# Kernel tuning notes

Hardware: AMD Instinct MI355X
Metric: run time of the kernel (lower is better)

Reference implementation:

```python
import jax, jax.numpy as jnp
import numpy as np

B, N, D = 2, 2048, 1024
H = 16
HD = D // H  # head_dim for kq and v

def setup_inputs() -> dict:
    key = jax.random.key(0)
    ks = jax.random.split(key, 5)
    scale = 1.0 / np.sqrt(D)
    return {
        "x": jax.random.normal(ks[0], (B, N, D), dtype=jnp.float32),
        "Wq": jax.random.normal(ks[1], (D, D), dtype=jnp.float32) * scale,
        "Wk": jax.random.normal(ks[2], (D, D), dtype=jnp.float32) * scale,
        "Wv": jax.random.normal(ks[3], (D, D), dtype=jnp.float32) * scale,
        "Wo": jax.random.normal(ks[4], (D, D), dtype=jnp.float32) * scale,
        "bo": jnp.zeros((D,), dtype=jnp.float32),
    }

def reference(x, Wq, Wk, Wv, Wo, bo):
    b, n, _ = x.shape
    # projections; torch Linear computes x @ W.T
    q = (x @ Wq.T).reshape(b, n, H, HD).transpose(0, 2, 1, 3)  # [B,H,N,HD]
    k = (x @ Wk.T).reshape(b, n, H, HD).transpose(0, 2, 1, 3)
    v = (x @ Wv.T).reshape(b, n, H, HD).transpose(0, 2, 1, 3)
    scores = jnp.einsum('bhqd,bhkd->bhqk', q, k) / jnp.sqrt(jnp.asarray(HD, x.dtype))
    causal = jnp.tril(jnp.ones((n, n), dtype=bool))
    scores = jnp.where(causal, scores, jnp.asarray(-jnp.inf, scores.dtype))
    probs = jax.nn.softmax(scores, axis=-1)  # dropout p=0.0 (eval)
    out = jnp.einsum('bhqk,bhkd->bhqd', probs, v)  # [B,H,N,HD]
    out = out.transpose(0, 2, 1, 3).reshape(b, n, D)
    return out @ Wo.T + bo
```

## Files before the change

kernel.cpp:

```cpp
#include <hip/hip_runtime.h>
#include <hip/hip_bf16.h>


typedef __bf16 bf16;
typedef __bf16 bf16x2 __attribute__((ext_vector_type(2)));
typedef __bf16 bf16x4 __attribute__((ext_vector_type(4)));
typedef __bf16 bf16x8 __attribute__((ext_vector_type(8)));
typedef float f32x4 __attribute__((ext_vector_type(4)));
typedef unsigned int u32x4 __attribute__((ext_vector_type(4)));

__device__ __forceinline__ f32x4 mfma16(bf16x8 a, bf16x8 b, f32x4 c) {
    return __builtin_amdgcn_mfma_f32_16x16x32_bf16(a, b, c, 0, 0, 0);
}

__device__ __forceinline__ void gload16(const bf16* g, bf16* l) {
    __builtin_amdgcn_global_load_lds(
        (const __attribute__((address_space(1))) unsigned int*)g,
        (__attribute__((address_space(3))) unsigned int*)l, 16, 0, 0);
}

__device__ __forceinline__ unsigned pk2(float a, float b) {
    bf16x2 v;
    v[0] = (bf16)a;
    v[1] = (bf16)b;
    return __builtin_bit_cast(unsigned, v);
}

__global__ __launch_bounds__(256) void f2b_kernel(const float* __restrict__ in,
                                                  bf16* __restrict__ out, int n) {
    int i = (blockIdx.x * 256 + threadIdx.x) * 4;
    if (i >= n) return;
    float4 v = *(const float4*)&in[i];
    bf16x4 o;
    o.x = (bf16)v.x; o.y = (bf16)v.y; o.z = (bf16)v.z; o.w = (bf16)v.w;
    *(bf16x4*)&out[i] = o;
}

__global__ __launch_bounds__(256) void w2b_kernel(
    const float* __restrict__ w0, const float* __restrict__ w1,
    const float* __restrict__ w2, const float* __restrict__ w3,
    bf16* __restrict__ o0, bf16* __restrict__ o1,
    bf16* __restrict__ o2, bf16* __restrict__ o3) {
    int sel = blockIdx.x >> 10;
    const float* in = sel == 0 ? w0 : sel == 1 ? w1 : sel == 2 ? w2 : w3;
    bf16* out = sel == 0 ? o0 : sel == 1 ? o1 : sel == 2 ? o2 : o3;
    int i = ((blockIdx.x & 1023) * 256 + threadIdx.x) * 4;
    float4 v = *(const float4*)&in[i];
    bf16x4 o;
    o.x = (bf16)v.x; o.y = (bf16)v.y; o.z = (bf16)v.z; o.w = (bf16)v.w;
    *(bf16x4*)&out[i] = o;
}

template <int MODE>
__device__ __forceinline__ void gemm_body(const bf16* __restrict__ A,
                                          const bf16* __restrict__ B,
                                          bf16* __restrict__ Cb,
                                          float* __restrict__ Cf,
                                          const float* __restrict__ bias,
                                          float scale, int N, int K, int row0, int col0) {
    __shared__ alignas(16) bf16 sA[128 * 32];
    __shared__ alignas(16) bf16 sB[128 * 32];
    const int tid  = threadIdx.x;
    const int lane = tid & 63;
    const int wave = tid >> 6;
    const int wrow = (wave >> 1) * 64;
    const int wcol = (wave & 1) * 64;
    const int la = lane & 15, lb = lane >> 4;

    const f32x4 fzero = {0.f, 0.f, 0.f, 0.f};
    f32x4 acc[4][4];
#pragma unroll
    for (int m = 0; m < 4; ++m)
#pragma unroll
        for (int n = 0; n < 4; ++n) acc[m][n] = fzero;

    for (int k0 = 0; k0 < K; k0 += 32) {
#pragma unroll
        for (int i = 0; i < 2; ++i) {
            int idx = i * 256 + tid;
            int r = idx >> 2, s = idx & 3;
            gload16(&A[(size_t)(row0 + r) * K + k0 + s * 8], &sA[idx * 8]);
            gload16(&B[(size_t)(col0 + r) * K + k0 + s * 8], &sB[idx * 8]);
        }
        __syncthreads();
        bf16x8 af[4], bfv[4];
#pragma unroll
        for (int m = 0; m < 4; ++m)
            af[m] = *(const bf16x8*)&sA[(wrow + m * 16 + la) * 32 + lb * 8];
#pragma unroll
        for (int n = 0; n < 4; ++n)
            bfv[n] = *(const bf16x8*)&sB[(wcol + n * 16 + la) * 32 + lb * 8];
#pragma unroll
        for (int m = 0; m < 4; ++m)
#pragma unroll
            for (int n = 0; n < 4; ++n)
                acc[m][n] = mfma16(af[m], bfv[n], acc[m][n]);
        __syncthreads();
    }
#pragma unroll
    for (int m = 0; m < 4; ++m)
#pragma unroll
        for (int n = 0; n < 4; ++n) {
            int col = col0 + wcol + n * 16 + la;
            if (MODE == 2) {
                int hh = col >> 6, hd = col & 63;
                int hc = hd >> 4, lav = hd & 15;
                int sp = row0 + wrow + m * 16 + lb * 4;
                int ktile = sp >> 6, k = sp & 63;
                int c = k >> 4, g = (k >> 2) & 3;
                size_t addr = (size_t)(ktile * 16 + hh) * 4096 +
                              (size_t)((hc * 2 + (c >> 1)) * 512 +
                                       (lav + g * 16) * 8 + (c & 1) * 4);
                bf16x4 o4;
#pragma unroll
                for (int r = 0; r < 4; ++r) o4[r] = (bf16)acc[m][n][r];
                *(bf16x4*)&Cb[addr] = o4;
            } else if (MODE == 3) {
                int hh = col >> 6, hd = col & 63;
#pragma unroll
                for (int r = 0; r < 4; ++r) {
                    int row = row0 + wrow + m * 16 + lb * 4 + r;
                    int ktile = row >> 6, key = row & 63;
                    size_t addr = (size_t)(ktile * 16 + hh) * 4096 +
                                  (size_t)(((key >> 4) * 2 + (hd >> 5)) * 512 +
                                           ((key & 15) + ((hd >> 3) & 3) * 16) * 8 +
                                           (hd & 7));
                    Cb[addr] = (bf16)acc[m][n][r];
                }
            } else {
#pragma unroll
                for (int r = 0; r < 4; ++r) {
                    int row = row0 + wrow + m * 16 + lb * 4 + r;
                    if (MODE == 1)
                        Cf[(size_t)row * N + col] = acc[m][n][r] + bias[col];
                    else
                        Cb[(size_t)row * N + col] = (bf16)(acc[m][n][r] * scale);
                }
            }
        }
}

__global__ __launch_bounds__(256) void gemm_qkv_kernel(
    const bf16* __restrict__ xb, const bf16* __restrict__ wq,
    const bf16* __restrict__ wk, const bf16* __restrict__ wv,
    bf16* __restrict__ Q, bf16* __restrict__ Kf, bf16* __restrict__ Vf) {
    int z = blockIdx.z;
    if (z == 2) {
        gemm_body<2>(xb, wv, Vf, nullptr, nullptr, 1.f, 1024, 1024,
                     blockIdx.x * 128, blockIdx.y * 128);
    } else if (z == 1) {
        gemm_body<3>(xb, wk, Kf, nullptr, nullptr, 1.f, 1024, 1024,
                     blockIdx.x * 128, blockIdx.y * 128);
    } else {
        gemm_body<0>(xb, wq, Q, nullptr, nullptr, 0.1803368801111204f, 1024, 1024,
                     blockIdx.x * 128, blockIdx.y * 128);
    }
}

__global__ __launch_bounds__(256) void gemm_out_kernel(
    const bf16* __restrict__ att, const bf16* __restrict__ wo,
    float* __restrict__ out, const float* __restrict__ bias) {
    gemm_body<1>(att, wo, nullptr, out, bias, 1.f, 1024, 1024,
                 blockIdx.x * 128, blockIdx.y * 128);
}

__global__ __launch_bounds__(256, 2) void attn_kernel(
    const bf16* __restrict__ Q, const bf16* __restrict__ Kf,
    const bf16* __restrict__ Vf, bf16* __restrict__ O) {
    __shared__ alignas(16) char smem[32768];
    const int lane = threadIdx.x & 63;
    const int wave = threadIdx.x >> 6;
    const int bid = blockIdx.x;
    const int bh = (bid & 7) * 4 + ((bid >> 3) & 3);
    const int slot = bid >> 5;
    const int qt = slot < 8 ? slot : 23 - slot;
    const int h = bh & 15;
    const int b = bh >> 4;
    const int q0w = qt * 128 + wave * 32;
    const int rowbase = b * 2048;
    const int la = lane & 15, lb = lane >> 4;
    const f32x4 fzero = {0.f, 0.f, 0.f, 0.f};
    const float C = 14.426950408889634f;
    const int colbase = h * 64;
    const size_t TSTRIDE = 16 * 4096;

    const bf16* kg = Kf + ((size_t)(b * 32) * 16 + h) * 4096 + lane * 8;
    const bf16* vg = Vf + ((size_t)(b * 32) * 16 + h) * 4096 + lane * 8;

    bf16x8 aq[2][2];
#pragma unroll
    for (int mf = 0; mf < 2; ++mf) {
        const bf16* qp = &Q[(size_t)(rowbase + q0w + mf * 16 + la) * 1024 + colbase];
#pragma unroll
        for (int kc = 0; kc < 2; ++kc) aq[mf][kc] = *(const bf16x8*)(qp + kc * 32 + lb * 8);
    }

    bf16x8 bones;
#pragma unroll
    for (int j = 0; j < 8; ++j) bones[j] = (bf16)1.0f;

    f32x4 o[2][4], lacc[2];
#pragma unroll
    for (int mf = 0; mf < 2; ++mf) {
        lacc[mf] = fzero;
#pragma unroll
        for (int hc = 0; hc < 4; ++hc) o[mf][hc] = fzero;
    }

    const int nt = (q0w + 95) >> 6;
    const int ntmax = 2 * qt + 2;

    auto STAGE = [&](int tile, int cur) {
        const bf16* ks = kg + (size_t)tile * TSTRIDE;
        const bf16* vs = vg + (size_t)tile * TSTRIDE;
        char* dst = smem + cur * 16384;
#pragma unroll
        for (int i = 0; i < 2; ++i) {
            int f = wave + i * 4;
            gload16(ks + f * 512, (bf16*)(dst + f * 1024));
            gload16(vs + f * 512, (bf16*)(dst + 8192 + f * 1024));
        }
    };

    STAGE(0, 0);
    __syncthreads();

    int cur = 0;
    for (int t = 0; t < ntmax; ++t) {
        if (t + 1 < ntmax) STAGE(t + 1, cur ^ 1);
        if (t < nt) {
            const char* kbuf = smem + cur * 16384;
            const char* vbuf = kbuf + 8192;
            f32x4 s[2][4];
#pragma unroll
            for (int mf = 0; mf < 2; ++mf)
#pragma unroll
                for (int ck = 0; ck < 4; ++ck) s[mf][ck] = fzero;
            __builtin_amdgcn_s_setprio(1);
#pragma unroll
            for (int ck = 0; ck < 4; ++ck) {
                bf16x8 k0 = *(const bf16x8*)(kbuf + (ck * 2 + 0) * 1024 + lane * 16);
                bf16x8 k1 = *(const bf16x8*)(kbuf + (ck * 2 + 1) * 1024 + lane * 16);
#pragma unroll
                for (int mf = 0; mf < 2; ++mf) {
                    s[mf][ck] = mfma16(k0, aq[mf][0], s[mf][ck]);
                    s[mf][ck] = mfma16(k1, aq[mf][1], s[mf][ck]);
                }
            }
            __builtin_amdgcn_s_setprio(0);
            if (t == nt - 1) {
                const int k0r = t * 64;
#pragma unroll
                for (int mf = 0; mf < 2; ++mf) {
                    int qrow = q0w + mf * 16 + la;
#pragma unroll
                    for (int ck = 0; ck < 4; ++ck)
#pragma unroll
                        for (int r = 0; r < 4; ++r) {
                            int key = k0r + ck * 16 + lb * 4 + r;
                            if (key > qrow) s[mf][ck][r] = -1e30f;
                        }
                }
            }
            bf16x8 pa[2][2];
#pragma unroll
            for (int mf = 0; mf < 2; ++mf) {
                unsigned pk[4][2];
#pragma unroll
                for (int ck = 0; ck < 4; ++ck) {
                    float p0 = __builtin_amdgcn_exp2f(s[mf][ck][0] - C);
                    float p1 = __builtin_amdgcn_exp2f(s[mf][ck][1] - C);
                    float p2 = __builtin_amdgcn_exp2f(s[mf][ck][2] - C);
                    float p3 = __builtin_amdgcn_exp2f(s[mf][ck][3] - C);
                    pk[ck][0] = pk2(p0, p1);
                    pk[ck][1] = pk2(p2, p3);
                }
#pragma unroll
                for (int kc2 = 0; kc2 < 2; ++kc2) {
                    u32x4 w;
                    w.x = pk[kc2 * 2][0];
                    w.y = pk[kc2 * 2][1];
                    w.z = pk[kc2 * 2 + 1][0];
                    w.w = pk[kc2 * 2 + 1][1];
                    pa[mf][kc2] = __builtin_bit_cast(bf16x8, w);
                }
            }
            __builtin_amdgcn_s_setprio(1);
#pragma unroll
            for (int hc = 0; hc < 4; ++hc) {
                bf16x8 v0 = *(const bf16x8*)(vbuf + (hc * 2 + 0) * 1024 + lane * 16);
                bf16x8 v1 = *(const bf16x8*)(vbuf + (hc * 2 + 1) * 1024 + lane * 16);
#pragma unroll
                for (int mf = 0; mf < 2; ++mf) {
                    o[mf][hc] = mfma16(pa[mf][0], v0, o[mf][hc]);
                    o[mf][hc] = mfma16(pa[mf][1], v1, o[mf][hc]);
                }
            }
#pragma unroll
            for (int mf = 0; mf < 2; ++mf) {
                lacc[mf] = mfma16(pa[mf][0], bones, lacc[mf]);
                lacc[mf] = mfma16(pa[mf][1], bones, lacc[mf]);
            }
            __builtin_amdgcn_s_setprio(0);
        }
        __syncthreads();
        cur ^= 1;
    }

#pragma unroll
    for (int mf = 0; mf < 2; ++mf)
#pragma unroll
        for (int hc = 0; hc < 4; ++hc)
#pragma unroll
            for (int r = 0; r < 4; ++r) {
                int qrow = q0w + mf * 16 + lb * 4 + r;
                O[(size_t)(rowbase + qrow) * 1024 + colbase + hc * 16 + la] =
                    (bf16)(o[mf][hc][r] / lacc[mf][r]);
            }
}

extern "C" void kernel_launch(void* const* d_in, const int* in_sizes, int n_in,
                              void* d_out, int out_size, void* d_ws, size_t ws_size,
                              hipStream_t stream) {
    const float* x  = (const float*)d_in[0];
    const float* Wq = (const float*)d_in[1];
    const float* Wk = (const float*)d_in[2];
    const float* Wv = (const float*)d_in[3];
    const float* Wo = (const float*)d_in[4];
    const float* bo = (const float*)d_in[5];
    float* out = (float*)d_out;

    char* ws = (char*)d_ws;
    const size_t MB = 1024 * 1024;
    bf16* xb  = (bf16*)(ws + (size_t)0);
    bf16* wqb = (bf16*)(ws + 8 * MB);
    bf16* wkb = (bf16*)(ws + 10 * MB);
    bf16* wvb = (bf16*)(ws + 12 * MB);
    bf16* wob = (bf16*)(ws + 14 * MB);
    bf16* Qb  = (bf16*)(ws + 16 * MB);
    bf16* Kf  = (bf16*)(ws + 24 * MB);
    bf16* Vf  = (bf16*)(ws + 40 * MB);
    bf16* Ab  = (bf16*)(ws + 56 * MB);

    f2b_kernel<<<4096, 256, 0, stream>>>(x, xb, 4096 * 1024);
    w2b_kernel<<<4096, 256, 0, stream>>>(Wq, Wk, Wv, Wo, wqb, wkb, wvb, wob);

    gemm_qkv_kernel<<<dim3(32, 8, 3), 256, 0, stream>>>(xb, wqb, wkb, wvb, Qb, Kf, Vf);
    attn_kernel<<<512, 256, 0, stream>>>(Qb, Kf, Vf, Ab);
    gemm_out_kernel<<<dim3(32, 8), 256, 0, stream>>>(Ab, wob, out, bo);
}
```

Baseline: 106.3 us.

## Double attention query tile per block and merge fp32-to-bf16 conversion kernels

The attention kernel now gives each block 256 query rows (64 per wave) instead of 128, so each staged K/V tile is reused across twice as many queries and the grid halves to 256 blocks. The causal load-balancing slot mapping is dropped, and the launch bound falls to one block per CU to make room for the larger register accumulators. The two conversion kernels are merged into a single launch to save one kernel launch. Risks include losing causal load balance, since blocks now have very different tile counts, and lower occupancy with only 256 blocks.

```diff
diff --git a/kernel.cpp b/kernel.cpp
--- a/kernel.cpp
+++ b/kernel.cpp
@@ -26,25 +26,25 @@
     return __builtin_bit_cast(unsigned, v);
 }
 
-__global__ __launch_bounds__(256) void f2b_kernel(const float* __restrict__ in,
-                                                  bf16* __restrict__ out, int n) {
-    int i = (blockIdx.x * 256 + threadIdx.x) * 4;
-    if (i >= n) return;
-    float4 v = *(const float4*)&in[i];
-    bf16x4 o;
-    o.x = (bf16)v.x; o.y = (bf16)v.y; o.z = (bf16)v.z; o.w = (bf16)v.w;
-    *(bf16x4*)&out[i] = o;
-}
-
-__global__ __launch_bounds__(256) void w2b_kernel(
-    const float* __restrict__ w0, const float* __restrict__ w1,
-    const float* __restrict__ w2, const float* __restrict__ w3,
+__global__ __launch_bounds__(256) void conv_kernel(
+    const float* __restrict__ x, const float* __restrict__ w0,
+    const float* __restrict__ w1, const float* __restrict__ w2,
+    const float* __restrict__ w3, bf16* __restrict__ xb,
     bf16* __restrict__ o0, bf16* __restrict__ o1,
     bf16* __restrict__ o2, bf16* __restrict__ o3) {
-    int sel = blockIdx.x >> 10;
-    const float* in = sel == 0 ? w0 : sel == 1 ? w1 : sel == 2 ? w2 : w3;
-    bf16* out = sel == 0 ? o0 : sel == 1 ? o1 : sel == 2 ? o2 : o3;
-    int i = ((blockIdx.x & 1023) * 256 + threadIdx.x) * 4;
+    int blk = blockIdx.x;
+    const float* in;
+    bf16* out;
+    int base;
+    if (blk < 4096) {
+        in = x; out = xb; base = blk;
+    } else {
+        int sel = (blk - 4096) >> 10;
+        in = sel == 0 ? w0 : sel == 1 ? w1 : sel == 2 ? w2 : w3;
+        out = sel == 0 ? o0 : sel == 1 ? o1 : sel == 2 ? o2 : o3;
+        base = (blk - 4096) & 1023;
+    }
+    int i = (base * 256 + threadIdx.x) * 4;
     float4 v = *(const float4*)&in[i];
     bf16x4 o;
     o.x = (bf16)v.x; o.y = (bf16)v.y; o.z = (bf16)v.z; o.w = (bf16)v.w;
@@ -164,7 +164,7 @@
                  blockIdx.x * 128, blockIdx.y * 128);
 }
 
-__global__ __launch_bounds__(256, 2) void attn_kernel(
+__global__ __launch_bounds__(256, 1) void attn_kernel(
     const bf16* __restrict__ Q, const bf16* __restrict__ Kf,
     const bf16* __restrict__ Vf, bf16* __restrict__ O) {
     __shared__ alignas(16) char smem[32768];
@@ -172,11 +172,10 @@
     const int wave = threadIdx.x >> 6;
     const int bid = blockIdx.x;
     const int bh = (bid & 7) * 4 + ((bid >> 3) & 3);
-    const int slot = bid >> 5;
-    const int qt = slot < 8 ? slot : 23 - slot;
+    const int qb = bid >> 5;
     const int h = bh & 15;
     const int b = bh >> 4;
-    const int q0w = qt * 128 + wave * 32;
+    const int q0w = qb * 256 + wave * 64;
     const int rowbase = b * 2048;
     const int la = lane & 15, lb = lane >> 4;
     const f32x4 fzero = {0.f, 0.f, 0.f, 0.f};
@@ -187,9 +186,9 @@
     const bf16* kg = Kf + ((size_t)(b * 32) * 16 + h) * 4096 + lane * 8;
     const bf16* vg = Vf + ((size_t)(b * 32) * 16 + h) * 4096 + lane * 8;
 
-    bf16x8 aq[2][2];
-#pragma unroll
-    for (int mf = 0; mf < 2; ++mf) {
+    bf16x8 aq[4][2];
+#pragma unroll
+    for (int mf = 0; mf < 4; ++mf) {
         const bf16* qp = &Q[(size_t)(rowbase + q0w + mf * 16 + la) * 1024 + colbase];
 #pragma unroll
         for (int kc = 0; kc < 2; ++kc) aq[mf][kc] = *(const bf16x8*)(qp + kc * 32 + lb * 8);
@@ -199,16 +198,16 @@
 #pragma unroll
     for (int j = 0; j < 8; ++j) bones[j] = (bf16)1.0f;
 
-    f32x4 o[2][4], lacc[2];
-#pragma unroll
-    for (int mf = 0; mf < 2; ++mf) {
+    f32x4 o[4][4], lacc[4];
+#pragma unroll
+    for (int mf = 0; mf < 4; ++mf) {
         lacc[mf] = fzero;
 #pragma unroll
         for (int hc = 0; hc < 4; ++hc) o[mf][hc] = fzero;
     }
 
-    const int nt = (q0w + 95) >> 6;
-    const int ntmax = 2 * qt + 2;
+    const int nt = 4 * qb + wave + 1;
+    const int ntmax = 4 * qb + 4;
 
     auto STAGE = [&](int tile, int cur) {
         const bf16* ks = kg + (size_t)tile * TSTRIDE;
@@ -231,47 +230,38 @@
         if (t < nt) {
             const char* kbuf = smem + cur * 16384;
             const char* vbuf = kbuf + 8192;
-            f32x4 s[2][4];
-#pragma unroll
-            for (int mf = 0; mf < 2; ++mf)
-#pragma unroll
-                for (int ck = 0; ck < 4; ++ck) s[mf][ck] = fzero;
+            bf16x8 pa[4][2];
             __builtin_amdgcn_s_setprio(1);
 #pragma unroll
-            for (int ck = 0; ck < 4; ++ck) {
-                bf16x8 k0 = *(const bf16x8*)(kbuf + (ck * 2 + 0) * 1024 + lane * 16);
-                bf16x8 k1 = *(const bf16x8*)(kbuf + (ck * 2 + 1) * 1024 + lane * 16);
-#pragma unroll
-                for (int mf = 0; mf < 2; ++mf) {
-                    s[mf][ck] = mfma16(k0, aq[mf][0], s[mf][ck]);
-                    s[mf][ck] = mfma16(k1, aq[mf][1], s[mf][ck]);
-                }
-            }
-            __builtin_amdgcn_s_setprio(0);
-            if (t == nt - 1) {
-                const int k0r = t * 64;
-#pragma unroll
-                for (int mf = 0; mf < 2; ++mf) {
+            for (int mf = 0; mf < 4; ++mf) {
+                f32x4 s[4];
+#pragma unroll
+                for (int ck = 0; ck < 4; ++ck) s[ck] = fzero;
+#pragma unroll
+                for (int ck = 0; ck < 4; ++ck) {
+                    bf16x8 k0 = *(const bf16x8*)(kbuf + (ck * 2 + 0) * 1024 + lane * 16);
+                    bf16x8 k1 = *(const bf16x8*)(kbuf + (ck * 2 + 1) * 1024 + lane * 16);
+                    s[ck] = mfma16(k0, aq[mf][0], s[ck]);
+                    s[ck] = mfma16(k1, aq[mf][1], s[ck]);
+                }
+                if (t == nt - 1) {
+                    const int k0r = t * 64;
                     int qrow = q0w + mf * 16 + la;
 #pragma unroll
                     for (int ck = 0; ck < 4; ++ck)
 #pragma unroll
                         for (int r = 0; r < 4; ++r) {
                             int key = k0r + ck * 16 + lb * 4 + r;
-                            if (key > qrow) s[mf][ck][r] = -1e30f;
+                            if (key > qrow) s[ck][r] = -1e30f;
                         }
                 }
-            }
-            bf16x8 pa[2][2];
-#pragma unroll
-            for (int mf = 0; mf < 2; ++mf) {
                 unsigned pk[4][2];
 #pragma unroll
                 for (int ck = 0; ck < 4; ++ck) {
-                    float p0 = __builtin_amdgcn_exp2f(s[mf][ck][0] - C);
-                    float p1 = __builtin_amdgcn_exp2f(s[mf][ck][1] - C);
-                    float p2 = __builtin_amdgcn_exp2f(s[mf][ck][2] - C);
-                    float p3 = __builtin_amdgcn_exp2f(s[mf][ck][3] - C);
+                    float p0 = __builtin_amdgcn_exp2f(s[ck][0] - C);
+                    float p1 = __builtin_amdgcn_exp2f(s[ck][1] - C);
+                    float p2 = __builtin_amdgcn_exp2f(s[ck][2] - C);
+                    float p3 = __builtin_amdgcn_exp2f(s[ck][3] - C);
                     pk[ck][0] = pk2(p0, p1);
                     pk[ck][1] = pk2(p2, p3);
                 }
@@ -285,19 +275,18 @@
                     pa[mf][kc2] = __builtin_bit_cast(bf16x8, w);
                 }
             }
-            __builtin_amdgcn_s_setprio(1);
 #pragma unroll
             for (int hc = 0; hc < 4; ++hc) {
                 bf16x8 v0 = *(const bf16x8*)(vbuf + (hc * 2 + 0) * 1024 + lane * 16);
                 bf16x8 v1 = *(const bf16x8*)(vbuf + (hc * 2 + 1) * 1024 + lane * 16);
 #pragma unroll
-                for (int mf = 0; mf < 2; ++mf) {
+                for (int mf = 0; mf < 4; ++mf) {
                     o[mf][hc] = mfma16(pa[mf][0], v0, o[mf][hc]);
                     o[mf][hc] = mfma16(pa[mf][1], v1, o[mf][hc]);
                 }
             }
 #pragma unroll
-            for (int mf = 0; mf < 2; ++mf) {
+            for (int mf = 0; mf < 4; ++mf) {
                 lacc[mf] = mfma16(pa[mf][0], bones, lacc[mf]);
                 lacc[mf] = mfma16(pa[mf][1], bones, lacc[mf]);
             }
@@ -308,7 +297,7 @@
     }
 
 #pragma unroll
-    for (int mf = 0; mf < 2; ++mf)
+    for (int mf = 0; mf < 4; ++mf)
 #pragma unroll
         for (int hc = 0; hc < 4; ++hc)
 #pragma unroll
@@ -342,10 +331,9 @@
     bf16* Vf  = (bf16*)(ws + 40 * MB);
     bf16* Ab  = (bf16*)(ws + 56 * MB);
 
-    f2b_kernel<<<4096, 256, 0, stream>>>(x, xb, 4096 * 1024);
-    w2b_kernel<<<4096, 256, 0, stream>>>(Wq, Wk, Wv, Wo, wqb, wkb, wvb, wob);
+    conv_kernel<<<8192, 256, 0, stream>>>(x, Wq, Wk, Wv, Wo, xb, wqb, wkb, wvb, wob);
 
     gemm_qkv_kernel<<<dim3(32, 8, 3), 256, 0, stream>>>(xb, wqb, wkb, wvb, Qb, Kf, Vf);
-    attn_kernel<<<512, 256, 0, stream>>>(Qb, Kf, Vf, Ab);
+    attn_kernel<<<256, 256, 0, stream>>>(Qb, Kf, Vf, Ab);
     gemm_out_kernel<<<dim3(32, 8), 256, 0, stream>>>(Ab, wob, out, bo);
 }
```

Result: slower. 131.6 us (+23.8%).
